# Kernel tuning notes

Measured on AMD Instinct MI355X. Metric: run time of the kernel, lower is better.

## Reference

```python
import jax, jax.numpy as jnp
import numpy as np

B, T, N = 32, 720, 321
K = 25        # moving-average kernel_size (init kwarg)
DEC_LEV = 3   # wavelet decomposition level (init kwarg)
F = 16        # sym8 filter length
A = 0.85      # soft-threshold shrink factor from the source

# pywt sym8 decomposition low-pass filter
_DEC_LO = np.array([
    -0.0033824159510061256, -0.00054213233179114812, 0.031695087811492981,
    0.0076074873249176054, -0.14329423835080971, -0.061273359067658524,
    0.48135965125837221, 0.77718575170052351, 0.36444189483533893,
    -0.051945838107709037, -0.027219029917056003, 0.049137179673607506,
    0.0038087520138906151, -0.014952258337048231, -0.0003029205147213668,
    0.0018899503327594609], dtype=np.float32)
_DEC_HI = (((-1.0) ** (np.arange(F) + 1)) * _DEC_LO[::-1]).astype(np.float32)
DEC_LO = jnp.asarray(_DEC_LO)
DEC_HI = jnp.asarray(_DEC_HI)
REC_LO = DEC_LO[::-1]
REC_HI = DEC_HI[::-1]


def _dwt(a):
    # single-level DWT, pywt 'symmetric' extension, downsample odd phase
    ext = jnp.pad(a, (F - 1, F - 1), mode='symmetric')
    ca = jnp.convolve(ext, DEC_LO, mode='valid')[1::2]
    cd = jnp.convolve(ext, DEC_HI, mode='valid')[1::2]
    return ca, cd


def _idwt(ca, cd):
    # upsample (zeros in odd slots), full conv with reconstruction filters, trim F-2
    L = ca.shape[0]
    up_a = jnp.zeros(2 * L - 1, ca.dtype).at[::2].set(ca)
    up_d = jnp.zeros(2 * L - 1, cd.dtype).at[::2].set(cd)
    rec = jnp.convolve(up_a, REC_LO) + jnp.convolve(up_d, REC_HI)
    return rec[F - 2: rec.shape[0] - (F - 2)]


def _denoise(sig):
    # wavedec -> universal soft-threshold (shrunk by A) on all detail levels -> waverec
    L = sig.shape[0]
    a = sig
    details = []  # details[0] = finest level cD1
    for _ in range(DEC_LEV):
        a, d = _dwt(a)
        details.append(d)
    sigma = jnp.median(jnp.abs(details[0])) / 0.6745
    lam = sigma * jnp.sqrt(jnp.float32(2.0 * np.log(float(L))))
    details = [jnp.where(jnp.abs(d) >= lam,
                         jnp.sign(d) * (jnp.abs(d) - A * lam),
                         jnp.zeros_like(d)) for d in details]
    for d in reversed(details):
        if a.shape[0] == d.shape[0] + 1:  # static-shape pywt length fixup
            a = a[:-1]
        a = _idwt(a, d)
    return a


def _moving_avg(x):
    # replicate-pad (K-1)//2 on both ends of time axis, then AvgPool1d(K, stride=1)
    p = (K - 1) // 2
    xp = jnp.concatenate([jnp.repeat(x[:, :1], p, axis=1), x,
                          jnp.repeat(x[:, -1:], p, axis=1)], axis=1)
    s = jax.lax.reduce_window(xp, 0.0, jax.lax.add, (1, K, 1), (1, 1, 1), 'VALID')
    return s / K


def _forward(x):
    trend = _moving_avg(x)            # [B,T,N]
    res = x - trend
    # T is even so the odd-length branch of the original is never taken
    trend_nn = _denoise(trend.reshape(-1)).reshape(x.shape)
    res_nn = _denoise(res.reshape(-1)).reshape(x.shape)
    return trend - trend_nn, trend_nn, res - res_nn, res_nn


def setup_inputs() -> dict:
    key = jax.random.key(0)
    return {"x": jax.random.normal(key, (B, T, N), dtype=jnp.float32)}


def reference(x):
    return _forward(x)
```

## Files before the change

### kernel.cpp

```cpp
#include <hip/hip_runtime.h>
#include <math.h>

#define BB 32
#define TT 720
#define NNN 321
#define KK 25
#define PP 12
#define TCH 24

constexpr int L0 = BB * TT * NNN;
constexpr int L1 = (L0 + 15) / 2;
constexpr int L2 = (L1 + 15) / 2;
constexpr int L3 = (L2 + 15) / 2;
constexpr unsigned KMED = (unsigned)((L1 - 1) / 2 + 1);
constexpr float AA = 0.85f;

constexpr int NH1B = 512;
constexpr int CH   = (L1 + NH1B - 1) / NH1B;
constexpr int CANDSZ = NH1B * CH;

#define NC3 1024
constexpr int LEN2T = 2 * NC3 + 32;
constexpr int LEN1T = 4 * NC3 + 80;
#define NF0 4096
constexpr int N1T = NF0 / 2 + 8;
constexpr int N2T = N1T / 2 + 7;
constexpr int NQ3 = (N2T + 1) / 2;

constexpr float DLO[16] = {
    -0.0033824159510061256f, -0.0005421323317911481f, 0.03169508781149298f,
    0.007607487324917605f,  -0.1432942383508097f,    -0.061273359067658524f,
    0.4813596512583722f,     0.7771857517005235f,     0.36444189483533895f,
    -0.05194583810770904f,  -0.027219029917056003f,   0.049137179673607506f,
    0.003808752013890615f,  -0.01495225833704823f,   -0.0003029205147213668f,
    0.0018899503327594609f };

__global__ void mavg_kernel(const float* __restrict__ x,
                            float* __restrict__ trend,
                            float* __restrict__ res) {
    constexpr int NCH = TT / TCH;
    int gid = blockIdx.x * blockDim.x + threadIdx.x;
    if (gid >= BB * NCH * NNN) return;
    int n    = gid % NNN;
    int rest = gid / NNN;
    int ch   = rest % NCH;
    int b    = rest / NCH;
    int t0   = ch * TCH;
    const float* xb = x + (size_t)b * TT * NNN + n;
    float sum = 0.f;
#pragma unroll
    for (int dt = -PP; dt <= PP; ++dt) {
        int tt = t0 + dt;
        tt = tt < 0 ? 0 : (tt >= TT ? TT - 1 : tt);
        sum += xb[(size_t)tt * NNN];
    }
    size_t base = (size_t)b * TT * NNN + (size_t)t0 * NNN + n;
    for (int i = 0; i < TCH; ++i) {
        int t = t0 + i;
        float tr = sum * (1.0f / (float)KK);
        size_t idx = base + (size_t)i * NNN;
        trend[idx] = tr;
        res[idx] = xb[(size_t)t * NNN] - tr;
        int tp = t + 1 + PP; if (tp > TT - 1) tp = TT - 1;
        int tm = t - PP;     if (tm < 0)      tm = 0;
        sum += xb[(size_t)tp * NNN] - xb[(size_t)tm * NNN];
    }
}

__global__ void dwt123_kernel(const float* __restrict__ trend,
                              const float* __restrict__ res,
                              float* __restrict__ cd1,
                              float* __restrict__ cd2,
                              float* __restrict__ ca3,
                              float* __restrict__ cd3,
                              unsigned* __restrict__ hist) {
    int s = blockIdx.y;
    int C0 = blockIdx.x * NC3;
    const float* a0 = s ? res : trend;
    __shared__ float s1[LEN1T];
    __shared__ float s2[LEN2T];
    __shared__ unsigned sh[4096];
    for (int b = threadIdx.x; b < 4096; b += 256) sh[b] = 0;
    __syncthreads();

    int T0 = 2 * C0 - 14;
    int S1 = 4 * C0 - 42; if (S1 < 0) S1 = 0;
    int E1 = 2 * (T0 + LEN2T) + 2; if (E1 > L1) E1 = L1;
    int len1 = E1 - S1;
    float* pcd1 = cd1 + (size_t)s * L1;

    int npair = (len1 + 1) / 2;
    for (int ip = threadIdx.x; ip < npair; ip += 256) {
        int i = 2 * ip;
        int o = S1 + i;
        float slo0, shi0, slo1, shi1;
        if (2 * o - 14 >= 0 && 2 * o + 3 < L0) {
            const float* p = a0 + 2 * o - 14;
            float v[18];
#pragma unroll
            for (int j = 0; j < 18; ++j) v[j] = p[j];
            slo0 = shi0 = slo1 = shi1 = 0.f;
#pragma unroll
            for (int j = 0; j < 16; ++j) {
                float h = (j & 1) ? DLO[15 - j] : -DLO[15 - j];
                slo0 = fmaf(DLO[j], v[15 - j], slo0);
                shi0 = fmaf(h,      v[15 - j], shi0);
                slo1 = fmaf(DLO[j], v[17 - j], slo1);
                shi1 = fmaf(h,      v[17 - j], shi1);
            }
        } else {
            float acc[2][2];
#pragma unroll
            for (int q = 0; q < 2; ++q) {
                int oo = o + q;
                float slo = 0.f, shi = 0.f;
                int bidx = 2 * oo + 1;
#pragma unroll
                for (int j = 0; j < 16; ++j) {
                    int idx = bidx - j;
                    if (idx < 0) idx = -1 - idx;
                    if (idx >= L0) idx = 2 * L0 - 1 - idx;
                    float v = a0[idx];
                    slo = fmaf(DLO[j], v, slo);
                    float h = (j & 1) ? DLO[15 - j] : -DLO[15 - j];
                    shi = fmaf(h, v, shi);
                }
                acc[q][0] = slo; acc[q][1] = shi;
            }
            slo0 = acc[0][0]; shi0 = acc[0][1];
            slo1 = acc[1][0]; shi1 = acc[1][1];
        }
        s1[i] = slo0;
        if (o >= 4 * C0 && o < 4 * C0 + 4 * NC3) {
            pcd1[o] = shi0;
            atomicAdd(&sh[__float_as_uint(fabsf(shi0)) >> 20], 1u);
        }
        if (i + 1 < len1) {
            s1[i + 1] = slo1;
            int o1 = o + 1;
            if (o1 >= 4 * C0 && o1 < 4 * C0 + 4 * NC3) {
                pcd1[o1] = shi1;
                atomicAdd(&sh[__float_as_uint(fabsf(shi1)) >> 20], 1u);
            }
        }
    }
    __syncthreads();

    for (int b = threadIdx.x; b < 4096; b += 256) {
        unsigned c = sh[b];
        if (c) atomicAdd(&hist[s * 4096 + b], c);
    }

    float* pcd2 = cd2 + (size_t)s * L2;
    for (int i = threadIdx.x; i < LEN2T; i += 256) {
        int e = T0 + i;
        if (e < 0 || e >= L2) continue;
        int base = 2 * e + 1;
        float slo = 0.f, shi = 0.f;
#pragma unroll
        for (int j = 0; j < 16; ++j) {
            int idx = base - j;
            if (idx < 0) idx = -1 - idx;
            if (idx >= L1) idx = 2 * L1 - 1 - idx;
            float v = s1[idx - S1];
            slo = fmaf(DLO[j], v, slo);
            float h = (j & 1) ? DLO[15 - j] : -DLO[15 - j];
            shi = fmaf(h, v, shi);
        }
        s2[i] = slo;
        if (e >= 2 * C0 && e < 2 * C0 + 2 * NC3) pcd2[e] = shi;
    }
    __syncthreads();
    for (int i = threadIdx.x; i < LEN2T; i += 256) {
        int e = T0 + i;
        if (e < 0)        s2[i] = s2[(-1 - e) - T0];
        else if (e >= L2) s2[i] = s2[(2 * L2 - 1 - e) - T0];
    }
    __syncthreads();
    float* pca3 = ca3 + (size_t)s * L3;
    float* pcd3 = cd3 + (size_t)s * L3;
    for (int i = threadIdx.x; i < NC3; i += 256) {
        int o = C0 + i;
        if (o >= L3) break;
        int b2 = 2 * o + 1 - T0;
        float slo = 0.f, shi = 0.f;
#pragma unroll
        for (int j = 0; j < 16; ++j) {
            float v = s2[b2 - j];
            slo = fmaf(DLO[j], v, slo);
            float h = (j & 1) ? DLO[15 - j] : -DLO[15 - j];
            shi = fmaf(h, v, shi);
        }
        pca3[o] = slo;
        pcd3[o] = shi;
    }
}

__device__ __forceinline__ float sthr(float d, float lam, float alam) {
    float ad = fabsf(d);
    return (ad >= lam) ? copysignf(ad - alam, d) : 0.f;
}

__global__ void idwt_fused(const float* __restrict__ ca3,
                           const float* __restrict__ cd3,
                           const float* __restrict__ cd2,
                           const float* __restrict__ cd1,
                           const float* __restrict__ trend,
                           const float* __restrict__ res,
                           float* __restrict__ out,
                           const float* __restrict__ lamArr) {
    int s = blockIdx.y;
    int F0 = blockIdx.x * NF0;
    float lam = lamArr[s], alam = AA * lam;
    const float* pa3 = ca3 + (size_t)s * L3;
    const float* pd3 = cd3 + (size_t)s * L3;
    const float* pd2 = cd2 + (size_t)s * L2;
    const float* pd1 = cd1 + (size_t)s * L1;
    __shared__ float r2[N2T + 1];
    __shared__ float r1[N1T];
    int A1 = F0 >> 1, A2 = F0 >> 2, Q3 = F0 >> 3;
    for (int i = threadIdx.x; i < NQ3; i += 256) {
        int q3 = Q3 + i;
        float a0 = 0.f, a1 = 0.f;
#pragma unroll
        for (int p = 0; p < 8; ++p) {
            int idx = q3 + p; if (idx > L3 - 1) idx = L3 - 1;
            float a = pa3[idx];
            float d = sthr(pd3[idx], lam, alam);
            a0 = fmaf(a, DLO[2 * p + 1], a0);
            a0 = fmaf(d, DLO[14 - 2 * p], a0);
            a1 = fmaf(a, DLO[2 * p], a1);
            a1 = fmaf(d, -DLO[15 - 2 * p], a1);
        }
        r2[2 * i] = a0; r2[2 * i + 1] = a1;
    }
    __syncthreads();
    for (int i = threadIdx.x; i < N1T / 2; i += 256) {
        int q2 = A2 + i;
        float a0 = 0.f, a1 = 0.f;
#pragma unroll
        for (int p = 0; p < 8; ++p) {
            float a = r2[i + p];
            int idx = q2 + p; if (idx > L2 - 1) idx = L2 - 1;
            float d = sthr(pd2[idx], lam, alam);
            a0 = fmaf(a, DLO[2 * p + 1], a0);
            a0 = fmaf(d, DLO[14 - 2 * p], a0);
            a1 = fmaf(a, DLO[2 * p], a1);
            a1 = fmaf(d, -DLO[15 - 2 * p], a1);
        }
        r1[2 * i] = a0; r1[2 * i + 1] = a1;
    }
    __syncthreads();
    const float* orig = s ? res : trend;
    float* o_diff = out + (size_t)(2 * s) * L0;
    float* o_nn   = out + (size_t)(2 * s + 1) * L0;
    for (int i = threadIdx.x; i < NF0 / 2; i += 256) {
        int q1 = A1 + i;
        int r0 = 2 * q1;
        if (r0 >= L0) break;
        float a0 = 0.f, a1 = 0.f;
#pragma unroll
        for (int p = 0; p < 8; ++p) {
            float a = r1[i + p];
            int idx = q1 + p; if (idx > L1 - 1) idx = L1 - 1;
            float d = sthr(pd1[idx], lam, alam);
            a0 = fmaf(a, DLO[2 * p + 1], a0);
            a0 = fmaf(d, DLO[14 - 2 * p], a0);
            a1 = fmaf(a, DLO[2 * p], a1);
            a1 = fmaf(d, -DLO[15 - 2 * p], a1);
        }
        float o0 = orig[r0], o1 = orig[r0 + 1];
        float2 nn; nn.x = a0; nn.y = a1;
        float2 df; df.x = o0 - a0; df.y = o1 - a1;
        *(float2*)(o_nn + r0)   = nn;
        *(float2*)(o_diff + r0) = df;
    }
}

__global__ void init_median(unsigned* __restrict__ hist,
                            unsigned* __restrict__ prefix,
                            unsigned* __restrict__ kArr) {
    int t = blockIdx.x * blockDim.x + threadIdx.x;
    if (t < 8192) hist[t] = 0;
    if (t < 2) { prefix[t] = 0; kArr[t] = KMED; }
}

__global__ void hist1_kernel(const float* __restrict__ d,
                             unsigned* __restrict__ hist,
                             const unsigned* __restrict__ prefix,
                             unsigned* __restrict__ cand,
                             unsigned* __restrict__ bcnt) {
    int s = blockIdx.y;
    int blk = blockIdx.x;
    const float* ds = d + (size_t)s * L1;
    unsigned* cs = cand + (size_t)s * CANDSZ + (size_t)blk * CH;
    __shared__ unsigned sh[4096];
    __shared__ unsigned slocal;
    for (int b = threadIdx.x; b < 4096; b += 256) sh[b] = 0;
    if (threadIdx.x == 0) slocal = 0;
    __syncthreads();
    unsigned pref = prefix[s] >> 20;
    int i0 = blk * CH;
    int i1 = i0 + CH; if (i1 > L1) i1 = L1;
    for (int i = i0 + threadIdx.x; i < i1; i += 256) {
        unsigned u = __float_as_uint(fabsf(ds[i]));
        if ((u >> 20) == pref) {
            atomicAdd(&sh[(u >> 8) & 0xFFFu], 1u);
            unsigned pos = atomicAdd(&slocal, 1u);
            cs[pos] = u;
        }
    }
    __syncthreads();
    if (threadIdx.x == 0) bcnt[s * NH1B + blk] = slocal;
    for (int b = threadIdx.x; b < 4096; b += 256) {
        unsigned c = sh[b];
        if (c) atomicAdd(&hist[s * 4096 + b], c);
    }
}

__global__ void hist2_kernel(const unsigned* __restrict__ cand,
                             unsigned* __restrict__ hist,
                             const unsigned* __restrict__ prefix,
                             const unsigned* __restrict__ bcnt) {
    int s = blockIdx.y;
    int blk = blockIdx.x;
    const unsigned* cs = cand + (size_t)s * CANDSZ + (size_t)blk * CH;
    __shared__ unsigned sh[256];
    sh[threadIdx.x] = 0;
    __syncthreads();
    unsigned pref = prefix[s] >> 8;
    unsigned n = bcnt[s * NH1B + blk];
    for (unsigned i = threadIdx.x; i < n; i += 256) {
        unsigned u = cs[i];
        if ((u >> 8) == pref) atomicAdd(&sh[u & 0xFFu], 1u);
    }
    __syncthreads();
    unsigned c = sh[threadIdx.x];
    if (c) atomicAdd(&hist[s * 4096 + threadIdx.x], c);
}

__global__ void select_kernel(unsigned* __restrict__ hist,
                              unsigned* __restrict__ prefix,
                              unsigned* __restrict__ kArr,
                              float* __restrict__ lamArr,
                              int nbins, int shift) {
    int s = blockIdx.x, t = threadIdx.x;
    int chunk = nbins >> 8;
    unsigned loc[16];
    unsigned* hs = hist + s * 4096 + t * chunk;
    unsigned csum = 0;
    for (int j = 0; j < chunk; ++j) { loc[j] = hs[j]; hs[j] = 0; csum += loc[j]; }
    unsigned v = csum;
    int lane = t & 63, wv = t >> 6;
#pragma unroll
    for (int off = 1; off < 64; off <<= 1) {
        unsigned u = (unsigned)__shfl_up((int)v, off, 64);
        if (lane >= off) v += u;
    }
    __shared__ unsigned wsum[4];
    if (lane == 63) wsum[wv] = v;
    __syncthreads();
    unsigned base = 0;
    for (int w2 = 0; w2 < wv; ++w2) base += wsum[w2];
    unsigned incl = base + v, excl = incl - csum;
    unsigned k = kArr[s];
    if (excl < k && incl >= k) {
        unsigned run = excl;
        for (int j = 0; j < chunk; ++j) {
            if (run < k && run + loc[j] >= k) {
                unsigned digit = (unsigned)(t * chunk + j);
                unsigned npref = prefix[s] | (digit << shift);
                prefix[s] = npref;
                kArr[s] = k - run;
                if (shift == 0) {
                    float med = __uint_as_float(npref);
                    lamArr[s] = (med / 0.6745f) * sqrtf(2.0f * logf((float)L0));
                }
                break;
            }
            run += loc[j];
        }
    }
}

extern "C" void kernel_launch(void* const* d_in, const int* in_sizes, int n_in,
                              void* d_out, int out_size, void* d_ws, size_t ws_size,
                              hipStream_t stream) {
    const float* x = (const float*)d_in[0];
    float* out = (float*)d_out;
    float* w = (float*)d_ws;

    float* trend = w;
    float* res   = w + (size_t)L0;
    float* cd1   = w + 2 * (size_t)L0;
    float* cd2   = cd1 + 2 * (size_t)L1;
    float* ca3   = cd2 + 2 * (size_t)L2;
    float* cd3   = ca3 + 2 * (size_t)L3;
    unsigned* cand   = (unsigned*)(cd3 + 2 * (size_t)L3);
    unsigned* hist   = cand + 2 * (size_t)CANDSZ;
    unsigned* prefix = hist + 8192;
    unsigned* kArr   = prefix + 2;
    float*    lamArr = (float*)(kArr + 2);
    unsigned* bcnt   = (unsigned*)(lamArr + 2);

    dim3 b256(256);

    init_median<<<32, b256, 0, stream>>>(hist, prefix, kArr);
    {
        int nthreads = BB * (TT / TCH) * NNN;
        mavg_kernel<<<(nthreads + 255) / 256, b256, 0, stream>>>(x, trend, res);
    }
    dwt123_kernel<<<dim3((L3 + NC3 - 1) / NC3, 2), b256, 0, stream>>>(
        trend, res, cd1, cd2, ca3, cd3, hist);
    select_kernel<<<2, b256, 0, stream>>>(hist, prefix, kArr, lamArr, 4096, 20);
    hist1_kernel<<<dim3(NH1B, 2), b256, 0, stream>>>(cd1, hist, prefix, cand, bcnt);
    select_kernel<<<2, b256, 0, stream>>>(hist, prefix, kArr, lamArr, 4096, 8);
    hist2_kernel<<<dim3(NH1B, 2), b256, 0, stream>>>(cand, hist, prefix, bcnt);
    select_kernel<<<2, b256, 0, stream>>>(hist, prefix, kArr, lamArr, 256, 0);

    idwt_fused<<<dim3((L0 + NF0 - 1) / NF0, 2), b256, 0, stream>>>(
        ca3, cd3, cd2, cd1, trend, res, out, lamArr);
}
```

Baseline: 299.3 us.

## Fold median select steps into last-block epilogues and widen idwt output stores

Removes the separate init and three select kernel launches. Initialization moves into mavg_kernel, and each select step runs in the last block to finish the preceding histogram kernel, detected with a threadfence plus an atomic done counter. The final idwt stage now computes two output pairs per thread, sharing the thresholded detail loads and using float4 loads and stores. This cuts launch gaps and memory transactions, at the cost of a serialized tail block in each histogram kernel and reliance on correct fence ordering.

```diff
diff --git a/kernel.cpp b/kernel.cpp
--- a/kernel.cpp
+++ b/kernel.cpp
@@ -35,11 +35,74 @@
     0.003808752013890615f,  -0.01495225833704823f,   -0.0003029205147213668f,
     0.0018899503327594609f };
 
+__device__ void select_body(unsigned* hist, unsigned* prefix, unsigned* kArr,
+                            float* lamArr, int nbins, int shift) {
+    int t = threadIdx.x;
+    int chunk = nbins >> 8;
+    __shared__ unsigned wsum[4];
+    for (int s = 0; s < 2; ++s) {
+        unsigned loc[16];
+        unsigned* hs = hist + s * 4096 + t * chunk;
+        unsigned csum = 0;
+        for (int j = 0; j < chunk; ++j) { loc[j] = atomicExch(&hs[j], 0u); csum += loc[j]; }
+        unsigned v = csum;
+        int lane = t & 63, wv = t >> 6;
+#pragma unroll
+        for (int off = 1; off < 64; off <<= 1) {
+            unsigned u = (unsigned)__shfl_up((int)v, off, 64);
+            if (lane >= off) v += u;
+        }
+        if (lane == 63) wsum[wv] = v;
+        __syncthreads();
+        unsigned base = 0;
+        for (int w2 = 0; w2 < wv; ++w2) base += wsum[w2];
+        unsigned incl = base + v, excl = incl - csum;
+        unsigned k = kArr[s];
+        if (excl < k && incl >= k) {
+            unsigned run = excl;
+            for (int j = 0; j < chunk; ++j) {
+                if (run < k && run + loc[j] >= k) {
+                    unsigned digit = (unsigned)(t * chunk + j);
+                    unsigned npref = prefix[s] | (digit << shift);
+                    prefix[s] = npref;
+                    kArr[s] = k - run;
+                    if (shift == 0) {
+                        float med = __uint_as_float(npref);
+                        lamArr[s] = (med / 0.6745f) * sqrtf(2.0f * logf((float)L0));
+                    }
+                    break;
+                }
+                run += loc[j];
+            }
+        }
+        __syncthreads();
+    }
+}
+
+__device__ bool i_am_last(unsigned* done, unsigned nBlocks) {
+    __shared__ int amLast;
+    __threadfence();
+    __syncthreads();
+    if (threadIdx.x == 0) {
+        unsigned prev = atomicAdd(done, 1u);
+        amLast = (prev == nBlocks - 1) ? 1 : 0;
+    }
+    __syncthreads();
+    return amLast != 0;
+}
+
 __global__ void mavg_kernel(const float* __restrict__ x,
                             float* __restrict__ trend,
-                            float* __restrict__ res) {
+                            float* __restrict__ res,
+                            unsigned* __restrict__ hist,
+                            unsigned* __restrict__ prefix,
+                            unsigned* __restrict__ kArr,
+                            unsigned* __restrict__ done) {
     constexpr int NCH = TT / TCH;
     int gid = blockIdx.x * blockDim.x + threadIdx.x;
+    if (gid < 8192) hist[gid] = 0;
+    if (gid < 2) { prefix[gid] = 0; kArr[gid] = KMED; }
+    if (gid < 3) done[gid] = 0;
     if (gid >= BB * NCH * NNN) return;
     int n    = gid % NNN;
     int rest = gid / NNN;
@@ -73,7 +136,11 @@
                               float* __restrict__ cd2,
                               float* __restrict__ ca3,
                               float* __restrict__ cd3,
-                              unsigned* __restrict__ hist) {
+                              unsigned* __restrict__ hist,
+                              unsigned* __restrict__ prefix,
+                              unsigned* __restrict__ kArr,
+                              float* __restrict__ lamArr,
+                              unsigned* __restrict__ done) {
     int s = blockIdx.y;
     int C0 = blockIdx.x * NC3;
     const float* a0 = s ? res : trend;
@@ -194,6 +261,9 @@
         pca3[o] = slo;
         pcd3[o] = shi;
     }
+
+    if (i_am_last(done + 0, gridDim.x * gridDim.y))
+        select_body(hist, prefix, kArr, lamArr, 4096, 20);
 }
 
 __device__ __forceinline__ float sthr(float d, float lam, float alam) {
@@ -254,42 +324,47 @@
     const float* orig = s ? res : trend;
     float* o_diff = out + (size_t)(2 * s) * L0;
     float* o_nn   = out + (size_t)(2 * s + 1) * L0;
-    for (int i = threadIdx.x; i < NF0 / 2; i += 256) {
-        int q1 = A1 + i;
+    for (int i = threadIdx.x; i < NF0 / 4; i += 256) {
+        int ii = 2 * i;
+        int q1 = A1 + ii;
         int r0 = 2 * q1;
         if (r0 >= L0) break;
-        float a0 = 0.f, a1 = 0.f;
+        float d[9];
+#pragma unroll
+        for (int p = 0; p < 9; ++p) {
+            int idx = q1 + p; if (idx > L1 - 1) idx = L1 - 1;
+            d[p] = sthr(pd1[idx], lam, alam);
+        }
+        float a0 = 0.f, a1 = 0.f, b0 = 0.f, b1 = 0.f;
 #pragma unroll
         for (int p = 0; p < 8; ++p) {
-            float a = r1[i + p];
-            int idx = q1 + p; if (idx > L1 - 1) idx = L1 - 1;
-            float d = sthr(pd1[idx], lam, alam);
-            a0 = fmaf(a, DLO[2 * p + 1], a0);
-            a0 = fmaf(d, DLO[14 - 2 * p], a0);
-            a1 = fmaf(a, DLO[2 * p], a1);
-            a1 = fmaf(d, -DLO[15 - 2 * p], a1);
-        }
-        float o0 = orig[r0], o1 = orig[r0 + 1];
-        float2 nn; nn.x = a0; nn.y = a1;
-        float2 df; df.x = o0 - a0; df.y = o1 - a1;
-        *(float2*)(o_nn + r0)   = nn;
-        *(float2*)(o_diff + r0) = df;
-    }
-}
-
-__global__ void init_median(unsigned* __restrict__ hist,
-                            unsigned* __restrict__ prefix,
-                            unsigned* __restrict__ kArr) {
-    int t = blockIdx.x * blockDim.x + threadIdx.x;
-    if (t < 8192) hist[t] = 0;
-    if (t < 2) { prefix[t] = 0; kArr[t] = KMED; }
+            float a  = r1[ii + p];
+            float ab = r1[ii + 1 + p];
+            a0 = fmaf(a,      DLO[2 * p + 1], a0);
+            a0 = fmaf(d[p],   DLO[14 - 2 * p], a0);
+            a1 = fmaf(a,      DLO[2 * p], a1);
+            a1 = fmaf(d[p],  -DLO[15 - 2 * p], a1);
+            b0 = fmaf(ab,     DLO[2 * p + 1], b0);
+            b0 = fmaf(d[p+1], DLO[14 - 2 * p], b0);
+            b1 = fmaf(ab,     DLO[2 * p], b1);
+            b1 = fmaf(d[p+1],-DLO[15 - 2 * p], b1);
+        }
+        float4 o4 = *(const float4*)(orig + r0);
+        float4 nn; nn.x = a0; nn.y = a1; nn.z = b0; nn.w = b1;
+        float4 df; df.x = o4.x - a0; df.y = o4.y - a1; df.z = o4.z - b0; df.w = o4.w - b1;
+        *(float4*)(o_nn + r0)   = nn;
+        *(float4*)(o_diff + r0) = df;
+    }
 }
 
 __global__ void hist1_kernel(const float* __restrict__ d,
                              unsigned* __restrict__ hist,
-                             const unsigned* __restrict__ prefix,
+                             unsigned* __restrict__ prefix,
                              unsigned* __restrict__ cand,
-                             unsigned* __restrict__ bcnt) {
+                             unsigned* __restrict__ bcnt,
+                             unsigned* __restrict__ kArr,
+                             float* __restrict__ lamArr,
+                             unsigned* __restrict__ done) {
     int s = blockIdx.y;
     int blk = blockIdx.x;
     const float* ds = d + (size_t)s * L1;
@@ -316,12 +391,17 @@
         unsigned c = sh[b];
         if (c) atomicAdd(&hist[s * 4096 + b], c);
     }
+    if (i_am_last(done + 1, gridDim.x * gridDim.y))
+        select_body(hist, prefix, kArr, lamArr, 4096, 8);
 }
 
 __global__ void hist2_kernel(const unsigned* __restrict__ cand,
                              unsigned* __restrict__ hist,
-                             const unsigned* __restrict__ prefix,
-                             const unsigned* __restrict__ bcnt) {
+                             unsigned* __restrict__ prefix,
+                             const unsigned* __restrict__ bcnt,
+                             unsigned* __restrict__ kArr,
+                             float* __restrict__ lamArr,
+                             unsigned* __restrict__ done) {
     int s = blockIdx.y;
     int blk = blockIdx.x;
     const unsigned* cs = cand + (size_t)s * CANDSZ + (size_t)blk * CH;
@@ -337,50 +417,8 @@
     __syncthreads();
     unsigned c = sh[threadIdx.x];
     if (c) atomicAdd(&hist[s * 4096 + threadIdx.x], c);
-}
-
-__global__ void select_kernel(unsigned* __restrict__ hist,
-                              unsigned* __restrict__ prefix,
-                              unsigned* __restrict__ kArr,
-                              float* __restrict__ lamArr,
-                              int nbins, int shift) {
-    int s = blockIdx.x, t = threadIdx.x;
-    int chunk = nbins >> 8;
-    unsigned loc[16];
-    unsigned* hs = hist + s * 4096 + t * chunk;
-    unsigned csum = 0;
-    for (int j = 0; j < chunk; ++j) { loc[j] = hs[j]; hs[j] = 0; csum += loc[j]; }
-    unsigned v = csum;
-    int lane = t & 63, wv = t >> 6;
-#pragma unroll
-    for (int off = 1; off < 64; off <<= 1) {
-        unsigned u = (unsigned)__shfl_up((int)v, off, 64);
-        if (lane >= off) v += u;
-    }
-    __shared__ unsigned wsum[4];
-    if (lane == 63) wsum[wv] = v;
-    __syncthreads();
-    unsigned base = 0;
-    for (int w2 = 0; w2 < wv; ++w2) base += wsum[w2];
-    unsigned incl = base + v, excl = incl - csum;
-    unsigned k = kArr[s];
-    if (excl < k && incl >= k) {
-        unsigned run = excl;
-        for (int j = 0; j < chunk; ++j) {
-            if (run < k && run + loc[j] >= k) {
-                unsigned digit = (unsigned)(t * chunk + j);
-                unsigned npref = prefix[s] | (digit << shift);
-                prefix[s] = npref;
-                kArr[s] = k - run;
-                if (shift == 0) {
-                    float med = __uint_as_float(npref);
-                    lamArr[s] = (med / 0.6745f) * sqrtf(2.0f * logf((float)L0));
-                }
-                break;
-            }
-            run += loc[j];
-        }
-    }
+    if (i_am_last(done + 2, gridDim.x * gridDim.y))
+        select_body(hist, prefix, kArr, lamArr, 256, 0);
 }
 
 extern "C" void kernel_launch(void* const* d_in, const int* in_sizes, int n_in,
@@ -402,22 +440,21 @@
     unsigned* kArr   = prefix + 2;
     float*    lamArr = (float*)(kArr + 2);
     unsigned* bcnt   = (unsigned*)(lamArr + 2);
+    unsigned* done   = bcnt + 2 * NH1B;
 
     dim3 b256(256);
 
-    init_median<<<32, b256, 0, stream>>>(hist, prefix, kArr);
     {
         int nthreads = BB * (TT / TCH) * NNN;
-        mavg_kernel<<<(nthreads + 255) / 256, b256, 0, stream>>>(x, trend, res);
+        mavg_kernel<<<(nthreads + 255) / 256, b256, 0, stream>>>(
+            x, trend, res, hist, prefix, kArr, done);
     }
     dwt123_kernel<<<dim3((L3 + NC3 - 1) / NC3, 2), b256, 0, stream>>>(
-        trend, res, cd1, cd2, ca3, cd3, hist);
-    select_kernel<<<2, b256, 0, stream>>>(hist, prefix, kArr, lamArr, 4096, 20);
-    hist1_kernel<<<dim3(NH1B, 2), b256, 0, stream>>>(cd1, hist, prefix, cand, bcnt);
-    select_kernel<<<2, b256, 0, stream>>>(hist, prefix, kArr, lamArr, 4096, 8);
-    hist2_kernel<<<dim3(NH1B, 2), b256, 0, stream>>>(cand, hist, prefix, bcnt);
-    select_kernel<<<2, b256, 0, stream>>>(hist, prefix, kArr, lamArr, 256, 0);
-
+        trend, res, cd1, cd2, ca3, cd3, hist, prefix, kArr, lamArr, done);
+    hist1_kernel<<<dim3(NH1B, 2), b256, 0, stream>>>(
+        cd1, hist, prefix, cand, bcnt, kArr, lamArr, done);
+    hist2_kernel<<<dim3(NH1B, 2), b256, 0, stream>>>(
+        cand, hist, prefix, bcnt, kArr, lamArr, done);
     idwt_fused<<<dim3((L0 + NF0 - 1) / NF0, 2), b256, 0, stream>>>(
         ca3, cd3, cd2, cd1, trend, res, out, lamArr);
 }
```

Result: slower. 589.8 us (+97.0%).
